# Kernel tuning notes

Hardware: AMD Instinct MI355X
Metric: run time of the kernel (lower is better)

## Reference

```python
import jax, jax.numpy as jnp
import numpy as np

N, E, G = 50000, 800000, 512
IN_DIM, HID, HEADS = 128, 32, 4
NEG_SLOPE = 0.2


def _gat_conv(x, W, a_src, a_dst, b, src, dst, heads, ch):
    # x: [N, F_in]; W: [F_in, heads*ch]; a_src/a_dst: [heads, ch]; b: [heads*ch]
    h = (x @ W).reshape(N, heads, ch)                      # [N,H,C]
    alpha_s = jnp.einsum('nhc,hc->nh', h, a_src)           # [N,H]
    alpha_d = jnp.einsum('nhc,hc->nh', h, a_dst)           # [N,H]
    e = jax.nn.leaky_relu(alpha_s[src] + alpha_d[dst], NEG_SLOPE)  # [E,H]
    # scatter-softmax over incoming edges of each destination node
    m = jax.ops.segment_max(e, dst, num_segments=N)        # [N,H]
    ex = jnp.exp(e - m[dst])
    denom = jax.ops.segment_sum(ex, dst, num_segments=N)   # [N,H]
    alpha = ex / (denom[dst] + 1e-16)                      # [E,H]
    msg = h[src] * alpha[:, :, None]                       # [E,H,C]
    out = jax.ops.segment_sum(msg, dst, num_segments=N)    # [N,H,C]
    return out.reshape(N, heads * ch) + b


def _forward(x, edge_index, batch_idx, params):
    # PyG GATConv default: add self-loops
    loops = jnp.arange(N, dtype=edge_index.dtype)
    src = jnp.concatenate([edge_index[0], loops])
    dst = jnp.concatenate([edge_index[1], loops])
    heads_per_layer = [(HEADS, HID), (HEADS, HID), (1, HID)]
    h = x
    for (W, a_s, a_d, b), (hh, cc) in zip(params, heads_per_layer):
        h = _gat_conv(h, W, a_s, a_d, b, src, dst, hh, cc)
        h = jax.nn.elu(h)  # dropout is identity in eval mode
    # global mean pool over graphs
    sums = jax.ops.segment_sum(h, batch_idx, num_segments=G)          # [G,HID]
    cnts = jax.ops.segment_sum(jnp.ones((N,), h.dtype), batch_idx, num_segments=G)
    return sums / jnp.maximum(cnts, 1.0)[:, None]


def setup_inputs() -> dict:
    key = jax.random.key(0)
    ks = jax.random.split(key, 16)
    x = jax.random.normal(ks[0], (N, IN_DIM), dtype=jnp.float32)
    edge_index = jax.random.randint(ks[1], (2, E), 0, N, dtype=jnp.int32)
    batch_idx = jnp.sort(jax.random.randint(ks[2], (N,), 0, G, dtype=jnp.int32))
    dims = [(IN_DIM, HEADS, HID), (HEADS * HID, HEADS, HID), (HEADS * HID, 1, HID)]
    inp = {'x': x, 'edge_index': edge_index, 'batch_idx': batch_idx}
    for i, (fin, hh, cc) in enumerate(dims, 1):
        s = 1.0 / np.sqrt(fin)
        inp[f'W{i}'] = jax.random.normal(ks[3 * i], (fin, hh * cc), jnp.float32) * s
        inp[f'as{i}'] = jax.random.normal(ks[3 * i + 1], (hh, cc), jnp.float32) * 0.1
        inp[f'ad{i}'] = jax.random.normal(ks[3 * i + 2], (hh, cc), jnp.float32) * 0.1
        inp[f'b{i}'] = jnp.zeros((hh * cc,), jnp.float32)
    return inp


def reference(x, edge_index, batch_idx, W1, as1, ad1, b1, W2, as2, ad2, b2, W3, as3, ad3, b3):
    params = [(W1, as1, ad1, b1), (W2, as2, ad2, b2), (W3, as3, ad3, b3)]
    return _forward(x, edge_index, batch_idx, params)
```

## Files before the change

### kernel.cpp

```cpp
#include <hip/hip_runtime.h>
#include <hip/hip_fp16.h>

#define THREADS 256
#define NREG 8
#define CAP 64

__device__ __forceinline__ float lrelu(float x) { return x > 0.f ? x : 0.2f * x; }
__device__ __forceinline__ float elu(float x) { return x > 0.f ? x : expm1f(x); }

template <int K, int H, int C>
__global__ __launch_bounds__(256, 4) void gemm_alpha_kernel(
    const float* __restrict__ X, const float* __restrict__ W,
    const float* __restrict__ a_src, const float* __restrict__ a_dst,
    __half* __restrict__ Hh, float* __restrict__ asb, float* __restrict__ adb, int nNodes) {
    constexpr int M = 128;
    constexpr int NB = 32;
    __shared__ float xs[NB][K + 4];

    const int t = threadIdx.x;
    const int wid = t >> 6;
    const int lane = t & 63;
    const int half = lane >> 5;
    const int lq = lane & 31;
    const int col4 = lq * 4;
    const int node0 = blockIdx.x * NB;
    const int nbase = node0 + wid * 8 + half * 4;

    for (int i = t; i < NB * K; i += THREADS) {
        int n = i >> 7, k = i & (K - 1);
        int gn = node0 + n;
        xs[n][k] = (gn < nNodes) ? X[(size_t)gn * K + k] : 0.f;
    }
    __syncthreads();

    float acc[4][4];
#pragma unroll
    for (int j = 0; j < 4; ++j)
#pragma unroll
        for (int c = 0; c < 4; ++c) acc[j][c] = 0.f;

    const int nloc = wid * 8 + half * 4;
    const float* wp = W + col4;

    float4 w4[4], w4n[4];
#pragma unroll
    for (int kk = 0; kk < 4; ++kk)
        w4[kk] = *reinterpret_cast<const float4*>(&wp[(size_t)kk * M]);

#pragma unroll 2
    for (int kg = 0; kg < K; kg += 4) {
        if (kg + 4 < K) {
#pragma unroll
            for (int kk = 0; kk < 4; ++kk)
                w4n[kk] = *reinterpret_cast<const float4*>(&wp[(size_t)(kg + 4 + kk) * M]);
        }
        float4 xv[4];
#pragma unroll
        for (int j = 0; j < 4; ++j)
            xv[j] = *reinterpret_cast<const float4*>(&xs[nloc + j][kg]);
#pragma unroll
        for (int kk = 0; kk < 4; ++kk) {
#pragma unroll
            for (int j = 0; j < 4; ++j) {
                float xj = (&xv[j].x)[kk];
                acc[j][0] += xj * w4[kk].x;
                acc[j][1] += xj * w4[kk].y;
                acc[j][2] += xj * w4[kk].z;
                acc[j][3] += xj * w4[kk].w;
            }
        }
#pragma unroll
        for (int kk = 0; kk < 4; ++kk) w4[kk] = w4n[kk];
    }

#pragma unroll
    for (int j = 0; j < 4; ++j) {
        int gn = nbase + j;
        if (gn < nNodes) {
            __half2 p01 = __floats2half2_rn(acc[j][0], acc[j][1]);
            __half2 p23 = __floats2half2_rn(acc[j][2], acc[j][3]);
            uint2 u = make_uint2(*reinterpret_cast<unsigned*>(&p01),
                                 *reinterpret_cast<unsigned*>(&p23));
            *reinterpret_cast<uint2*>(&Hh[(size_t)gn * M + col4]) = u;
        }
    }

    float as_[4], ad_[4];
#pragma unroll
    for (int c = 0; c < 4; ++c) { as_[c] = a_src[col4 + c]; ad_[c] = a_dst[col4 + c]; }

    float sv[4], dv[4];
#pragma unroll
    for (int j = 0; j < 4; ++j) {
        sv[j] = acc[j][0] * as_[0] + acc[j][1] * as_[1] + acc[j][2] * as_[2] +
                acc[j][3] * as_[3];
        dv[j] = acc[j][0] * ad_[0] + acc[j][1] * ad_[1] + acc[j][2] * ad_[2] +
                acc[j][3] * ad_[3];
    }
#pragma unroll
    for (int off = 1; off < 8; off <<= 1) {
#pragma unroll
        for (int j = 0; j < 4; ++j) {
            sv[j] += __shfl_xor(sv[j], off);
            dv[j] += __shfl_xor(dv[j], off);
        }
    }
    if ((lq & 7) == 0) {
        int h = lq >> 3;
#pragma unroll
        for (int j = 0; j < 4; ++j) {
            int gn = nbase + j;
            if (gn < nNodes) {
                asb[gn * H + h] = sv[j];
                adb[gn * H + h] = dv[j];
            }
        }
    }
}

template <int K>
__global__ void gemm32_alpha_kernel(const float* __restrict__ X, const float* __restrict__ W,
                                    const float* __restrict__ a_src,
                                    const float* __restrict__ a_dst,
                                    __half* __restrict__ Hh, float* __restrict__ asb,
                                    float* __restrict__ adb, int nNodes) {
    constexpr int M = 32;
    constexpr int NB = 16;
    constexpr int NL = THREADS / M;
    constexpr int PER = NB / NL;
    __shared__ float xs[NB][K];

    int node0 = blockIdx.x * NB;
    for (int i = threadIdx.x; i < NB * K; i += THREADS) {
        int nn = i / K, kk = i % K;
        int n = node0 + nn;
        xs[nn][kk] = (n < nNodes) ? X[(size_t)n * K + kk] : 0.f;
    }
    __syncthreads();

    int col = threadIdx.x & 31;
    int nl = threadIdx.x >> 5;
    float acc[PER];
#pragma unroll
    for (int i = 0; i < PER; ++i) acc[i] = 0.f;

    for (int k = 0; k < K; ++k) {
        float w = W[k * M + col];
#pragma unroll
        for (int i = 0; i < PER; ++i) acc[i] += xs[nl + i * NL][k] * w;
    }

    float as = a_src[col], ad = a_dst[col];
#pragma unroll
    for (int i = 0; i < PER; ++i) {
        int n = node0 + nl + i * NL;
        float sv = acc[i] * as, dv = acc[i] * ad;
#pragma unroll
        for (int off = 1; off < 32; off <<= 1) {
            sv += __shfl_xor(sv, off);
            dv += __shfl_xor(dv, off);
        }
        if (n < nNodes) {
            Hh[(size_t)n * M + col] = __float2half(acc[i]);
            if (col == 0) { asb[n] = sv; adb[n] = dv; }
        }
    }
}

__global__ void scatterP_kernel(const int* __restrict__ src, const int* __restrict__ dst,
                                int* __restrict__ cursor, unsigned short* __restrict__ csr,
                                int nE, int N) {
    const int r = blockIdx.x & (NREG - 1);
    const int nb = gridDim.x / NREG;
    const int bi = blockIdx.x / NREG;
    const int span = (N + NREG - 1) / NREG;
    const int lo = r * span;
    const int hi = min(N, lo + span);
    const int stride = nb * THREADS;
    for (int e = bi * THREADS + (int)threadIdx.x; e < nE; e += stride) {
        int d = dst[e];
        if (d >= lo && d < hi) {
            int p = atomicAdd(&cursor[d], 1);
            if (p < CAP) csr[(d << 6) + p] = (unsigned short)src[e];
        }
    }
}

template <int H>
__device__ __forceinline__ void load_t(const float* __restrict__ asb, int s, bool valid,
                                       const float* adn, float* t) {
    if constexpr (H == 4) {
        float4 a4 = reinterpret_cast<const float4*>(asb)[s];
        float v[4] = {a4.x, a4.y, a4.z, a4.w};
#pragma unroll
        for (int h = 0; h < 4; ++h) t[h] = valid ? lrelu(v[h] + adn[h]) : -3.0e38f;
    } else {
        t[0] = valid ? lrelu(asb[s] + adn[0]) : -3.0e38f;
    }
}

template <int M, int H, int C>
__global__ void node_aggr(const __half* __restrict__ Hh, const float* __restrict__ asb,
                          const float* __restrict__ adb, const int* __restrict__ degArr,
                          const unsigned short* __restrict__ csr,
                          const float* __restrict__ bias, float* __restrict__ out,
                          int nNodes) {
    constexpr int WPB = THREADS / 64;
    constexpr int PSTR = (H == 4) ? 5 : 1;
    __shared__ uint2 pair_sh[WPB][64 * PSTR];

    const int wid = threadIdx.x >> 6;
    const int lane = threadIdx.x & 63;
    const int node = blockIdx.x * WPB + wid;
    if (node >= nNodes) return;

    const int e0 = node << 6;
    const int deg = min(degArr[node], CAP);

    float adn[H], eself[H];
    if constexpr (H == 4) {
        float4 ad4 = reinterpret_cast<const float4*>(adb)[node];
        float4 as4 = reinterpret_cast<const float4*>(asb)[node];
        adn[0] = ad4.x; adn[1] = ad4.y; adn[2] = ad4.z; adn[3] = ad4.w;
        eself[0] = lrelu(as4.x + adn[0]);
        eself[1] = lrelu(as4.y + adn[1]);
        eself[2] = lrelu(as4.z + adn[2]);
        eself[3] = lrelu(as4.w + adn[3]);
    } else {
        adn[0] = adb[node];
        eself[0] = lrelu(asb[node] + adn[0]);
    }

    const bool valid = lane < deg;
    const int s = valid ? (int)csr[e0 + lane] : node;
    float t[H];
    load_t<H>(asb, s, valid, adn, t);

    float ex[H], den[H], inv[H];
#pragma unroll
    for (int h = 0; h < H; ++h) { ex[h] = __expf(t[h]); den[h] = ex[h]; }
#pragma unroll
    for (int off = 32; off > 0; off >>= 1)
#pragma unroll
        for (int h = 0; h < H; ++h) den[h] += __shfl_xor(den[h], off);
#pragma unroll
    for (int h = 0; h < H; ++h) {
        den[h] += __expf(eself[h]);
        inv[h] = 1.f / (den[h] + 1e-16f);
    }

    unsigned wo = (unsigned)(s * M);
#pragma unroll
    for (int h = 0; h < H; ++h) {
        float al = ex[h] * inv[h];
        pair_sh[wid][lane * PSTR + h] = make_uint2(wo, __float_as_uint(al));
    }

    if constexpr (M == 128) {
        constexpr int CPL = 2;
        int ch = lane * CPL;
        const int myh = ch / C;

        float ii = inv[0], es = eself[0];
#pragma unroll
        for (int h = 1; h < H; ++h)
            if (myh == h) { ii = inv[h]; es = eself[h]; }

        float acc[2];
        const float alSelf = __expf(es) * ii;
        float2 hv0 = __half22float2(
            *reinterpret_cast<const __half2*>(&Hh[(size_t)node * M + ch]));
        acc[0] = alSelf * hv0.x;
        acc[1] = alSelf * hv0.y;

        int cnt = (deg + 7) & ~7;
        for (int j0 = 0; j0 < cnt; j0 += 8) {
#pragma unroll
            for (int jj = 0; jj < 8; ++jj) {
                int j = j0 + jj;
                uint2 p = pair_sh[wid][j * PSTR + myh];
                float al = __uint_as_float(p.y);
                __half2 h2 = *reinterpret_cast<const __half2*>(&Hh[(int)p.x + ch]);
                float2 hv = __half22float2(h2);
                acc[0] += al * hv.x;
                acc[1] += al * hv.y;
            }
        }

#pragma unroll
        for (int c = 0; c < 2; ++c)
            out[(size_t)node * M + ch + c] = elu(acc[c] + bias[ch + c]);
    } else {
        const int g2 = lane >> 5;
        const int c = lane & 31;
        const float ii = inv[0], es = eself[0];

        float acc = 0.f;
        int cnt = (deg + 15) & ~15;
        for (int j0 = 0; j0 < cnt; j0 += 16) {
#pragma unroll
            for (int jj = 0; jj < 8; ++jj) {
                int j = j0 + jj * 2 + g2;
                uint2 p = pair_sh[wid][j];
                float al = __uint_as_float(p.y);
                acc += al * __half2float(Hh[(int)p.x + c]);
            }
        }

        acc += __shfl_xor(acc, 32);
        if (lane < 32) {
            const float alSelf = __expf(es) * ii;
            float sv = __half2float(Hh[(size_t)node * M + c]);
            out[(size_t)node * M + c] = elu(acc + alSelf * sv + bias[c]);
        }
    }
}

__global__ void pool_kernel(const float* __restrict__ act, const int* __restrict__ batch,
                            float* __restrict__ out, int N, int G) {
    int wid = threadIdx.x >> 6;
    int lane = threadIdx.x & 63;
    int g = blockIdx.x * (THREADS / 64) + wid;
    if (g >= G) return;

    int s, e;
    {
        int lo = 0, hi = N;
        while (lo < hi) { int mid = (lo + hi) >> 1; if (batch[mid] < g) lo = mid + 1; else hi = mid; }
        s = lo;
        hi = N;
        while (lo < hi) { int mid = (lo + hi) >> 1; if (batch[mid] < g + 1) lo = mid + 1; else hi = mid; }
        e = lo;
    }

    int c = lane & 31, half = lane >> 5;
    float acc = 0.f;
    for (int n = s + half; n < e; n += 2) acc += act[(size_t)n * 32 + c];
    acc += __shfl_xor(acc, 32);
    if (lane < 32) out[g * 32 + c] = acc / fmaxf((float)(e - s), 1.f);
}

extern "C" void kernel_launch(void* const* d_in, const int* in_sizes, int n_in, void* d_out,
                              int out_size, void* d_ws, size_t ws_size, hipStream_t stream) {
    const float* x = (const float*)d_in[0];
    const int* ei = (const int*)d_in[1];
    const int* batch = (const int*)d_in[2];
    const float* W1 = (const float*)d_in[3];
    const float* as1 = (const float*)d_in[4];
    const float* ad1 = (const float*)d_in[5];
    const float* b1 = (const float*)d_in[6];
    const float* W2 = (const float*)d_in[7];
    const float* as2 = (const float*)d_in[8];
    const float* ad2 = (const float*)d_in[9];
    const float* b2 = (const float*)d_in[10];
    const float* W3 = (const float*)d_in[11];
    const float* as3 = (const float*)d_in[12];
    const float* ad3 = (const float*)d_in[13];
    const float* b3 = (const float*)d_in[14];

    const int N = in_sizes[0] / 128;
    const int E = in_sizes[1] / 2;
    const int G = out_size / 32;
    const int* srcp = ei;
    const int* dstp = ei + E;

    char* ws = (char*)d_ws;
    float* B = (float*)ws;
    __half* Hh = (__half*)(B + (size_t)N * 128);
    float* asb = (float*)(Hh + (size_t)N * 128);
    float* adb = asb + (size_t)N * 4;
    int* cursor = (int*)(adb + (size_t)N * 4);
    unsigned short* csr = (unsigned short*)(cursor + N);

    const int scatterBlocks = NREG * 256;
    const int gaBlocks = (N + 31) / 32;

    hipMemsetAsync(cursor, 0, (size_t)N * 4, stream);
    scatterP_kernel<<<scatterBlocks, THREADS, 0, stream>>>(srcp, dstp, cursor, csr, E, N);

    gemm_alpha_kernel<128, 4, 32><<<gaBlocks, THREADS, 0, stream>>>(x, W1, as1, ad1, Hh, asb,
                                                                    adb, N);
    node_aggr<128, 4, 32><<<(N + 3) / 4, THREADS, 0, stream>>>(Hh, asb, adb, cursor, csr, b1,
                                                               B, N);
    gemm_alpha_kernel<128, 4, 32><<<gaBlocks, THREADS, 0, stream>>>(B, W2, as2, ad2, Hh, asb,
                                                                    adb, N);
    node_aggr<128, 4, 32><<<(N + 3) / 4, THREADS, 0, stream>>>(Hh, asb, adb, cursor, csr, b2,
                                                               B, N);
    gemm32_alpha_kernel<128><<<(N + 15) / 16, THREADS, 0, stream>>>(B, W3, as3, ad3, Hh, asb,
                                                                    adb, N);
    node_aggr<32, 1, 32><<<(N + 3) / 4, THREADS, 0, stream>>>(Hh, asb, adb, cursor, csr, b3,
                                                              B, N);

    pool_kernel<<<(G + 3) / 4, THREADS, 0, stream>>>(B, batch, (float*)d_out, N, G);
}
```

Measured before the change: 266.6 us.

## Enlarge GEMM node tile to 64 and double-buffer weight loads in two halves

The 128-wide GEMM+alpha kernel now processes 64 nodes per block, with each thread computing 8 nodes by 4 columns instead of 4 by 4. This reuses each loaded weight float4 across twice as many nodes. The k-loop now steps by 8 and keeps two weight register sets, prefetching the next set while the other is used. In exchange it raises register and shared-memory use per block (LDS roughly doubles), which may lower occupancy under the 256,4 launch bounds. It also halves the number of blocks.

```diff
diff --git a/kernel.cpp b/kernel.cpp
--- a/kernel.cpp
+++ b/kernel.cpp
@@ -14,7 +14,7 @@
     const float* __restrict__ a_src, const float* __restrict__ a_dst,
     __half* __restrict__ Hh, float* __restrict__ asb, float* __restrict__ adb, int nNodes) {
     constexpr int M = 128;
-    constexpr int NB = 32;
+    constexpr int NB = 64;
     __shared__ float xs[NB][K + 4];
 
     const int t = threadIdx.x;
@@ -24,7 +24,8 @@
     const int lq = lane & 31;
     const int col4 = lq * 4;
     const int node0 = blockIdx.x * NB;
-    const int nbase = node0 + wid * 8 + half * 4;
+    const int nloc = wid * 16 + half * 8;
+    const int nbase = node0 + nloc;
 
     for (int i = t; i < NB * K; i += THREADS) {
         int n = i >> 7, k = i & (K - 1);
@@ -33,48 +34,71 @@
     }
     __syncthreads();
 
-    float acc[4][4];
-#pragma unroll
-    for (int j = 0; j < 4; ++j)
+    float acc[8][4];
+#pragma unroll
+    for (int j = 0; j < 8; ++j)
 #pragma unroll
         for (int c = 0; c < 4; ++c) acc[j][c] = 0.f;
 
-    const int nloc = wid * 8 + half * 4;
     const float* wp = W + col4;
-
-    float4 w4[4], w4n[4];
+    float4 wA[4], wB[4];
 #pragma unroll
     for (int kk = 0; kk < 4; ++kk)
-        w4[kk] = *reinterpret_cast<const float4*>(&wp[(size_t)kk * M]);
+        wA[kk] = *reinterpret_cast<const float4*>(&wp[(size_t)kk * M]);
+#pragma unroll
+    for (int kk = 0; kk < 4; ++kk)
+        wB[kk] = *reinterpret_cast<const float4*>(&wp[(size_t)(4 + kk) * M]);
 
 #pragma unroll 2
-    for (int kg = 0; kg < K; kg += 4) {
-        if (kg + 4 < K) {
-#pragma unroll
-            for (int kk = 0; kk < 4; ++kk)
-                w4n[kk] = *reinterpret_cast<const float4*>(&wp[(size_t)(kg + 4 + kk) * M]);
-        }
-        float4 xv[4];
-#pragma unroll
-        for (int j = 0; j < 4; ++j)
-            xv[j] = *reinterpret_cast<const float4*>(&xs[nloc + j][kg]);
-#pragma unroll
-        for (int kk = 0; kk < 4; ++kk) {
-#pragma unroll
-            for (int j = 0; j < 4; ++j) {
-                float xj = (&xv[j].x)[kk];
-                acc[j][0] += xj * w4[kk].x;
-                acc[j][1] += xj * w4[kk].y;
-                acc[j][2] += xj * w4[kk].z;
-                acc[j][3] += xj * w4[kk].w;
-            }
-        }
-#pragma unroll
-        for (int kk = 0; kk < 4; ++kk) w4[kk] = w4n[kk];
-    }
-
-#pragma unroll
-    for (int j = 0; j < 4; ++j) {
+    for (int kg = 0; kg < K; kg += 8) {
+        {
+            float4 xv[8];
+#pragma unroll
+            for (int j = 0; j < 8; ++j)
+                xv[j] = *reinterpret_cast<const float4*>(&xs[nloc + j][kg]);
+#pragma unroll
+            for (int kk = 0; kk < 4; ++kk) {
+#pragma unroll
+                for (int j = 0; j < 8; ++j) {
+                    float xj = (&xv[j].x)[kk];
+                    acc[j][0] += xj * wA[kk].x;
+                    acc[j][1] += xj * wA[kk].y;
+                    acc[j][2] += xj * wA[kk].z;
+                    acc[j][3] += xj * wA[kk].w;
+                }
+            }
+            if (kg + 8 < K) {
+#pragma unroll
+                for (int kk = 0; kk < 4; ++kk)
+                    wA[kk] = *reinterpret_cast<const float4*>(&wp[(size_t)(kg + 8 + kk) * M]);
+            }
+        }
+        {
+            float4 xv[8];
+#pragma unroll
+            for (int j = 0; j < 8; ++j)
+                xv[j] = *reinterpret_cast<const float4*>(&xs[nloc + j][kg + 4]);
+#pragma unroll
+            for (int kk = 0; kk < 4; ++kk) {
+#pragma unroll
+                for (int j = 0; j < 8; ++j) {
+                    float xj = (&xv[j].x)[kk];
+                    acc[j][0] += xj * wB[kk].x;
+                    acc[j][1] += xj * wB[kk].y;
+                    acc[j][2] += xj * wB[kk].z;
+                    acc[j][3] += xj * wB[kk].w;
+                }
+            }
+            if (kg + 12 < K) {
+#pragma unroll
+                for (int kk = 0; kk < 4; ++kk)
+                    wB[kk] = *reinterpret_cast<const float4*>(&wp[(size_t)(kg + 12 + kk) * M]);
+            }
+        }
+    }
+
+#pragma unroll
+    for (int j = 0; j < 8; ++j) {
         int gn = nbase + j;
         if (gn < nNodes) {
             __half2 p01 = __floats2half2_rn(acc[j][0], acc[j][1]);
@@ -89,9 +113,9 @@
 #pragma unroll
     for (int c = 0; c < 4; ++c) { as_[c] = a_src[col4 + c]; ad_[c] = a_dst[col4 + c]; }
 
-    float sv[4], dv[4];
-#pragma unroll
-    for (int j = 0; j < 4; ++j) {
+    float sv[8], dv[8];
+#pragma unroll
+    for (int j = 0; j < 8; ++j) {
         sv[j] = acc[j][0] * as_[0] + acc[j][1] * as_[1] + acc[j][2] * as_[2] +
                 acc[j][3] * as_[3];
         dv[j] = acc[j][0] * ad_[0] + acc[j][1] * ad_[1] + acc[j][2] * ad_[2] +
@@ -100,7 +124,7 @@
 #pragma unroll
     for (int off = 1; off < 8; off <<= 1) {
 #pragma unroll
-        for (int j = 0; j < 4; ++j) {
+        for (int j = 0; j < 8; ++j) {
             sv[j] += __shfl_xor(sv[j], off);
             dv[j] += __shfl_xor(dv[j], off);
         }
@@ -108,7 +132,7 @@
     if ((lq & 7) == 0) {
         int h = lq >> 3;
 #pragma unroll
-        for (int j = 0; j < 4; ++j) {
+        for (int j = 0; j < 8; ++j) {
             int gn = nbase + j;
             if (gn < nNodes) {
                 asb[gn * H + h] = sv[j];
@@ -373,7 +397,7 @@
     unsigned short* csr = (unsigned short*)(cursor + N);
 
     const int scatterBlocks = NREG * 256;
-    const int gaBlocks = (N + 31) / 32;
+    const int gaBlocks = (N + 63) / 64;
 
     hipMemsetAsync(cursor, 0, (size_t)N * 4, stream);
     scatterP_kernel<<<scatterBlocks, THREADS, 0, stream>>>(srcp, dstp, cursor, csr, E, N);
```

Result: slower. 887.4 us (+232.9%).
